# Kernel tuning notes

Measured on AMD Instinct MI355X. Metric: run time of the kernel, lower is better.

Reference implementation:

```python
import jax, jax.numpy as jnp
import numpy as np

B, S, D = 8, 2048, 512

def setup_inputs() -> dict:
    key = jax.random.key(0)
    k1, k2, k3 = jax.random.split(key, 3)
    context = jax.random.normal(k1, (B, S, D), dtype=jnp.float32)
    # nn.Linear default init ~ U(-1/sqrt(D), 1/sqrt(D)); scale keeps softmax sane
    bound = 1.0 / np.sqrt(D)
    W_in = jax.random.uniform(k2, (D, D), dtype=jnp.float32, minval=-bound, maxval=bound)
    W_out = jax.random.uniform(k3, (D, D), dtype=jnp.float32, minval=-bound, maxval=bound)
    return {"context": context, "W_in": W_in, "W_out": W_out}

def reference(context, W_in, W_out):
    # linear_in: x @ W_in.T (torch Linear convention)
    c = jnp.einsum('bsd,ed->bse', context, W_in)            # [B,S,D]
    scores = jnp.einsum('bsd,btd->bst', c, c)               # [B,S,S], no 1/sqrt(d) scale
    attn = jax.nn.softmax(scores, axis=-1)                  # [B,S,S]
    ctx = jnp.einsum('bst,btd->bsd', attn, c)               # [B,S,D]
    out = jnp.einsum('bsd,ed->bse', jnp.tanh(ctx), W_out)   # linear_out
    return out, attn
```

## Files before the change

### kernel.cpp

```cpp
#include <hip/hip_runtime.h>
#include <cstdint>
#include <cstddef>

#define Bc 8
#define Sc 2048
#define Dc 512

typedef float f32x4 __attribute__((ext_vector_type(4)));
typedef __bf16 bf16x8 __attribute__((ext_vector_type(8)));
typedef __bf16 bf16x4 __attribute__((ext_vector_type(4)));

__device__ __forceinline__ void gload_lds16(const void* g, void* l) {
    __builtin_amdgcn_global_load_lds((const __attribute__((address_space(1))) void*)g,
                                     (__attribute__((address_space(3))) void*)l, 16, 0, 0);
}

__device__ __forceinline__ f32x4 mfma16x16x32(bf16x8 a, bf16x8 b, f32x4 c) {
    return __builtin_amdgcn_mfma_f32_16x16x32_bf16(a, b, c, 0, 0, 0);
}

__global__ void k_convert_w(const float* __restrict__ wi, const float* __restrict__ wo,
                            __bf16* __restrict__ wib, __bf16* __restrict__ wob) {
    int i = blockIdx.x * 256 + threadIdx.x;
    wib[i] = (__bf16)wi[i];
    wob[i] = (__bf16)wo[i];
}

__global__ __launch_bounds__(256) void k_scores(
        const __bf16* __restrict__ c, __bf16* __restrict__ Ebuf,
        float2* __restrict__ stats)
{
    __shared__ alignas(16) char smem[34816];
    __bf16* As = (__bf16*)smem;
    __bf16* Bs = (__bf16*)(smem + 16384);
    const int tid  = threadIdx.x;
    const int wave = tid >> 6, lane = tid & 63;
    const int waveM = wave >> 1, waveN = wave & 1;
    const int bid  = blockIdx.x;
    const int bz   = bid & 7;
    const int col0 = ((bid >> 3) & 15) * 128;
    const int row0 = (bid >> 7) * 128;
    const __bf16* A  = c + (size_t)bz * Sc * Dc;

    f32x4 acc[4][4] = {};

    for (int k0 = 0; k0 < Dc; k0 += 64) {
        #pragma unroll
        for (int i = 0; i < 4; ++i) {
            int flat = i * 2048 + wave * 512 + lane * 8;
            int r  = flat >> 6;
            int cc = (flat >> 3) & 7;
            int gc = (cc ^ (r & 7)) << 3;
            gload_lds16(A + (size_t)(row0 + r) * Dc + k0 + gc, As + i * 2048 + wave * 512);
            gload_lds16(A + (size_t)(col0 + r) * Dc + k0 + gc, Bs + i * 2048 + wave * 512);
        }
        __syncthreads();
        #pragma unroll
        for (int ks = 0; ks < 2; ++ks) {
            const int kc = ks * 4 + (lane >> 4);
            bf16x8 av[4], bv[4];
            #pragma unroll
            for (int mi = 0; mi < 4; ++mi) {
                int r = waveM * 64 + mi * 16 + (lane & 15);
                av[mi] = *(const bf16x8*)&As[r * 64 + ((kc ^ (r & 7)) << 3)];
            }
            #pragma unroll
            for (int ni = 0; ni < 4; ++ni) {
                int r = waveN * 64 + ni * 16 + (lane & 15);
                bv[ni] = *(const bf16x8*)&Bs[r * 64 + ((kc ^ (r & 7)) << 3)];
            }
            #pragma unroll
            for (int mi = 0; mi < 4; ++mi)
                #pragma unroll
                for (int ni = 0; ni < 4; ++ni)
                    acc[mi][ni] = mfma16x16x32(av[mi], bv[ni], acc[mi][ni]);
        }
        __syncthreads();
    }

    const int rb = (lane >> 4) << 2;
    const int cb = lane & 15;
    __bf16* Es = (__bf16*)smem;
    #pragma unroll
    for (int mi = 0; mi < 4; ++mi)
        #pragma unroll
        for (int rr = 0; rr < 4; ++rr) {
            float mx = fmaxf(fmaxf(acc[mi][0][rr], acc[mi][1][rr]),
                             fmaxf(acc[mi][2][rr], acc[mi][3][rr]));
            #pragma unroll
            for (int off = 1; off < 16; off <<= 1) mx = fmaxf(mx, __shfl_xor(mx, off));
            const int rloc = waveM * 64 + mi * 16 + rb + rr;
            float zs = 0.f;
            #pragma unroll
            for (int ni = 0; ni < 4; ++ni) {
                float e = __expf(acc[mi][ni][rr] - mx);
                zs += e;
                Es[rloc * 136 + waveN * 64 + ni * 16 + cb] = (__bf16)e;
            }
            #pragma unroll
            for (int off = 1; off < 16; off <<= 1) zs += __shfl_xor(zs, off);
            if ((lane & 15) == 0)
                stats[((size_t)bz * Sc + row0 + rloc) * 32 + (col0 >> 6) + waveN] =
                    make_float2(mx, zs);
        }
    __syncthreads();
    #pragma unroll
    for (int p = 0; p < 8; ++p) {
        int r  = p * 16 + (tid >> 4);
        int cc = (tid & 15) * 8;
        bf16x8 v = *(const bf16x8*)&Es[r * 136 + cc];
        *(bf16x8*)&Ebuf[((size_t)bz * Sc + row0 + r) * Sc + col0 + cc] = v;
    }
}

__global__ __launch_bounds__(256) void k_combine(const float2* __restrict__ stats,
                                                 float* __restrict__ corrTab) {
    int r = blockIdx.x * 256 + threadIdx.x;
    float2 s[32];
    #pragma unroll
    for (int i = 0; i < 32; ++i) s[i] = stats[(size_t)r * 32 + i];
    float M = s[0].x;
    #pragma unroll
    for (int i = 1; i < 32; ++i) M = fmaxf(M, s[i].x);
    float Z = 0.f;
    #pragma unroll
    for (int i = 0; i < 32; ++i) Z += s[i].y * __expf(s[i].x - M);
    float zi = 1.f / Z;
    #pragma unroll
    for (int i = 0; i < 32; ++i) corrTab[(size_t)r * 32 + i] = __expf(s[i].x - M) * zi;
}

__global__ __launch_bounds__(512, 4) void k_pv_fused(
        const __bf16* __restrict__ Buf,
        const __bf16* __restrict__ cT,
        const float* __restrict__ corrTab,
        float* __restrict__ attn,
        __bf16* __restrict__ ctx)
{
    __shared__ alignas(16) __bf16 As[32 * 64];
    __shared__ alignas(16) __bf16 Bs[512 * 64];
    const int tid  = threadIdx.x;
    const int wave = tid >> 6, lane = tid & 63;
    const int b    = blockIdx.x & 7;
    const int row0 = (blockIdx.x >> 3) * 32;
    const __bf16* Bt = cT + (size_t)b * Dc * Sc;

    const int ar = tid >> 4;
    const int ac = (tid & 15) * 4;
    const __bf16* erow = Buf + ((size_t)b * Sc + row0 + ar) * Sc + ac;
    const float*  crow = corrTab + ((size_t)b * Sc + row0 + ar) * 32;
    float*        prow = attn + ((size_t)b * Sc + row0 + ar) * Sc + ac;
    const int a_addr = ar * 64 + (((ac >> 3) ^ (ar & 7)) << 3) + (ac & 4);

    f32x4 acc[2][4] = {};
    const int NT = Sc / 64;

    auto stageB = [&](int kt) {
        #pragma unroll
        for (int i = 0; i < 8; ++i) {
            int chunk = i * 512 + wave * 64 + lane;
            int r  = chunk >> 3;
            int cc = chunk & 7;
            gload_lds16(Bt + (size_t)r * Sc + kt + ((cc ^ (r & 7)) << 3),
                        Bs + (size_t)chunk * 8);
        }
    };

    bf16x4 e_cur = *(const bf16x4*)&erow[0];
    float  c_cur = crow[0];

    for (int t = 0; t < NT; ++t) {
        stageB(t * 64);
        f32x4 p;
        #pragma unroll
        for (int j = 0; j < 4; ++j) p[j] = (float)e_cur[j] * c_cur;
        bf16x4 pb;
        #pragma unroll
        for (int j = 0; j < 4; ++j) pb[j] = (__bf16)p[j];
        *(bf16x4*)&As[a_addr] = pb;
        __syncthreads();
        *(f32x4*)&prow[t * 64] = p;
        if (t + 1 < NT) {
            e_cur = *(const bf16x4*)&erow[(t + 1) * 64];
            c_cur = crow[t + 1];
        }
        const int kcb = lane >> 4;
        #pragma unroll
        for (int ks = 0; ks < 2; ++ks) {
            const int kc = ks * 4 + kcb;
            bf16x8 av[2], bv[4];
            #pragma unroll
            for (int mi = 0; mi < 2; ++mi) {
                int r = mi * 16 + (lane & 15);
                av[mi] = *(const bf16x8*)&As[r * 64 + ((kc ^ (r & 7)) << 3)];
            }
            #pragma unroll
            for (int ni = 0; ni < 4; ++ni) {
                int r = wave * 64 + ni * 16 + (lane & 15);
                bv[ni] = *(const bf16x8*)&Bs[r * 64 + ((kc ^ (r & 7)) << 3)];
            }
            #pragma unroll
            for (int mi = 0; mi < 2; ++mi)
                #pragma unroll
                for (int ni = 0; ni < 4; ++ni)
                    acc[mi][ni] = mfma16x16x32(av[mi], bv[ni], acc[mi][ni]);
        }
        __syncthreads();
    }

    const int rb = (lane >> 4) << 2;
    const int cb = lane & 15;
    #pragma unroll
    for (int mi = 0; mi < 2; ++mi)
        #pragma unroll
        for (int ni = 0; ni < 4; ++ni) {
            int gr = row0 + mi * 16 + rb;
            int gc = wave * 64 + ni * 16 + cb;
            #pragma unroll
            for (int rr = 0; rr < 4; ++rr)
                ctx[(size_t)(b * Sc + gr + rr) * Dc + gc] = (__bf16)tanhf(acc[mi][ni][rr]);
        }
}

__global__ __launch_bounds__(256) void k_gemm_bf16(
        const __bf16* __restrict__ A, const __bf16* __restrict__ Bt,
        float* __restrict__ C, int lda, int ldb, int ldc, int K)
{
    __shared__ alignas(16) __bf16 smem[2 * 128 * 64];
    __bf16* As = smem;
    __bf16* Bs = smem + 128 * 64;
    const int tid  = threadIdx.x;
    const int wave = tid >> 6, lane = tid & 63;
    const int waveM = wave >> 1, waveN = wave & 1;
    const int row0 = blockIdx.y * 128;
    const int col0 = blockIdx.x * 128;

    f32x4 acc[4][4] = {};

    for (int k0 = 0; k0 < K; k0 += 64) {
        #pragma unroll
        for (int i = 0; i < 4; ++i) {
            int flat = i * 2048 + wave * 512 + lane * 8;
            int r  = flat >> 6;
            int cc = (flat >> 3) & 7;
            int gc = (cc ^ (r & 7)) << 3;
            gload_lds16(A  + (size_t)(row0 + r) * lda + k0 + gc, As + i * 2048 + wave * 512);
            gload_lds16(Bt + (size_t)(col0 + r) * ldb + k0 + gc, Bs + i * 2048 + wave * 512);
        }
        __syncthreads();
        #pragma unroll
        for (int ks = 0; ks < 2; ++ks) {
            const int kc = ks * 4 + (lane >> 4);
            bf16x8 av[4], bv[4];
            #pragma unroll
            for (int mi = 0; mi < 4; ++mi) {
                int r = waveM * 64 + mi * 16 + (lane & 15);
                av[mi] = *(const bf16x8*)&As[r * 64 + ((kc ^ (r & 7)) << 3)];
            }
            #pragma unroll
            for (int ni = 0; ni < 4; ++ni) {
                int r = waveN * 64 + ni * 16 + (lane & 15);
                bv[ni] = *(const bf16x8*)&Bs[r * 64 + ((kc ^ (r & 7)) << 3)];
            }
            #pragma unroll
            for (int mi = 0; mi < 4; ++mi)
                #pragma unroll
                for (int ni = 0; ni < 4; ++ni)
                    acc[mi][ni] = mfma16x16x32(av[mi], bv[ni], acc[mi][ni]);
        }
        __syncthreads();
    }

    const int rb = (lane >> 4) << 2;
    const int cb = lane & 15;
    #pragma unroll
    for (int mi = 0; mi < 4; ++mi)
        #pragma unroll
        for (int ni = 0; ni < 4; ++ni) {
            int gr = row0 + waveM * 64 + mi * 16 + rb;
            int gc = col0 + waveN * 64 + ni * 16 + cb;
            #pragma unroll
            for (int rr = 0; rr < 4; ++rr)
                C[(size_t)(gr + rr) * ldc + gc] = acc[mi][ni][rr];
        }
}

__global__ __launch_bounds__(256) void k_cproj(
        const float* __restrict__ A, const __bf16* __restrict__ Bt,
        __bf16* __restrict__ Cb, __bf16* __restrict__ CTb)
{
    __shared__ alignas(16) char smem[49152];
    float*  Asf = (float*)smem;
    __bf16* Bs  = (__bf16*)(smem + 32768);
    const int tid  = threadIdx.x;
    const int wave = tid >> 6, lane = tid & 63;
    const int waveM = wave >> 1, waveN = wave & 1;
    const int row0 = blockIdx.y * 128;
    const int col0 = blockIdx.x * 128;

    f32x4 acc[4][4] = {};

    for (int k0 = 0; k0 < Dc; k0 += 64) {
        #pragma unroll
        for (int i = 0; i < 8; ++i) {
            int flat = i * 1024 + wave * 256 + lane * 4;
            int r  = flat >> 6;
            int cc = (flat >> 2) & 15;
            int gc = (cc ^ (r & 15)) << 2;
            gload_lds16(A + (size_t)(row0 + r) * Dc + k0 + gc, Asf + i * 1024 + wave * 256);
        }
        #pragma unroll
        for (int i = 0; i < 4; ++i) {
            int flat = i * 2048 + wave * 512 + lane * 8;
            int r  = flat >> 6;
            int cc = (flat >> 3) & 7;
            int gc = (cc ^ (r & 7)) << 3;
            gload_lds16(Bt + (size_t)(col0 + r) * Dc + k0 + gc, Bs + i * 2048 + wave * 512);
        }
        __syncthreads();
        #pragma unroll
        for (int ks = 0; ks < 2; ++ks) {
            const int kc8 = ks * 4 + (lane >> 4);
            const int kc4 = kc8 << 1;
            bf16x8 av[4], bv[4];
            #pragma unroll
            for (int mi = 0; mi < 4; ++mi) {
                int r  = waveM * 64 + mi * 16 + (lane & 15);
                int r4 = r & 15;
                f32x4 lo = *(const f32x4*)&Asf[r * 64 + (((kc4    ) ^ r4) << 2)];
                f32x4 hi = *(const f32x4*)&Asf[r * 64 + (((kc4 + 1) ^ r4) << 2)];
                bf16x8 a;
                a[0] = (__bf16)lo[0]; a[1] = (__bf16)lo[1]; a[2] = (__bf16)lo[2]; a[3] = (__bf16)lo[3];
                a[4] = (__bf16)hi[0]; a[5] = (__bf16)hi[1]; a[6] = (__bf16)hi[2]; a[7] = (__bf16)hi[3];
                av[mi] = a;
            }
            #pragma unroll
            for (int ni = 0; ni < 4; ++ni) {
                int r = waveN * 64 + ni * 16 + (lane & 15);
                bv[ni] = *(const bf16x8*)&Bs[r * 64 + ((kc8 ^ (r & 7)) << 3)];
            }
            #pragma unroll
            for (int mi = 0; mi < 4; ++mi)
                #pragma unroll
                for (int ni = 0; ni < 4; ++ni)
                    acc[mi][ni] = mfma16x16x32(av[mi], bv[ni], acc[mi][ni]);
        }
        __syncthreads();
    }

    const int rb = (lane >> 4) << 2;
    const int cb = lane & 15;
    __bf16* T = (__bf16*)smem;
    #pragma unroll
    for (int mi = 0; mi < 4; ++mi)
        #pragma unroll
        for (int ni = 0; ni < 4; ++ni) {
            int lr = waveM * 64 + mi * 16 + rb;
            int lc = waveN * 64 + ni * 16 + cb;
            #pragma unroll
            for (int rr = 0; rr < 4; ++rr) {
                __bf16 h = (__bf16)acc[mi][ni][rr];
                Cb[(size_t)(row0 + lr + rr) * Dc + col0 + lc] = h;
                T[lc * 136 + lr + rr] = h;
            }
        }
    __syncthreads();
    const int bb = row0 >> 11;
    const int s0 = row0 & 2047;
    #pragma unroll
    for (int i = 0; i < 8; ++i) {
        int n  = i * 16 + (tid >> 4);
        int mo = (tid & 15) * 8;
        bf16x8 v = *(const bf16x8*)&T[n * 136 + mo];
        *(bf16x8*)&CTb[(size_t)bb * Dc * Sc + (size_t)(col0 + n) * Sc + s0 + mo] = v;
    }
}

extern "C" void kernel_launch(void* const* d_in, const int* in_sizes, int n_in,
                              void* d_out, int out_size, void* d_ws, size_t ws_size,
                              hipStream_t stream)
{
    (void)in_sizes; (void)n_in; (void)out_size; (void)ws_size;
    const float* context = (const float*)d_in[0];
    const float* W_in    = (const float*)d_in[1];
    const float* W_out   = (const float*)d_in[2];
    float* out  = (float*)d_out;
    float* attn = out + (size_t)Bc * Sc * Dc;

    char* ws = (char*)d_ws;
    __bf16* c_bf    = (__bf16*)ws;
    __bf16* cT_bf   = (__bf16*)(ws + 16777216);
    __bf16* wi_bf   = (__bf16*)(ws + 33554432);
    __bf16* wo_bf   = (__bf16*)(ws + 34078720);
    float2* stats   = (float2*)(ws + 34603008);
    float*  corrTab = (float*)(ws + 38797312);
    __bf16* Ebuf    = (__bf16*)(ws + 40894464);

    k_convert_w<<<dim3(Dc * Dc / 256), 256, 0, stream>>>(W_in, W_out, wi_bf, wo_bf);

    k_cproj<<<dim3(Dc / 128, (Bc * Sc) / 128), 256, 0, stream>>>(context, wi_bf, c_bf, cT_bf);

    k_scores<<<dim3(Bc * 16 * 16), 256, 0, stream>>>(c_bf, Ebuf, stats);

    k_combine<<<dim3(Bc * Sc / 256), 256, 0, stream>>>(stats, corrTab);

    k_pv_fused<<<dim3((Sc / 32) * Bc), 512, 0, stream>>>(Ebuf, cT_bf, corrTab, attn, c_bf);

    k_gemm_bf16<<<dim3(Dc / 128, (Bc * Sc) / 128, 1), 256, 0, stream>>>(
        c_bf, wo_bf, out, Dc, Dc, Dc, Dc);
}
```

Measured before the change: 189.7 us.

## Pre-convert context to bf16 and retile PV kernel into 64-row, half-D blocks

Adds a separate pass that converts the fp32 context to bf16, so the projection GEMM stages bf16 tiles directly instead of fp32 tiles converted in registers. The fused PV kernel is retiled from 32 rows by the full D with 512 threads to 64 rows by half of D with 256 threads. Only the first half-D block writes the attn output, and each block reads the E rows once per 256 columns. The aim is a lower LDS footprint and more MFMA work per staged B tile, at the cost of an extra 32MB of traffic for the conversion and reading Ebuf twice.

```diff
diff --git a/kernel.cpp b/kernel.cpp
--- a/kernel.cpp
+++ b/kernel.cpp
@@ -24,6 +24,96 @@
     int i = blockIdx.x * 256 + threadIdx.x;
     wib[i] = (__bf16)wi[i];
     wob[i] = (__bf16)wo[i];
+}
+
+__global__ __launch_bounds__(256) void k_convert_x(const float* __restrict__ x,
+                                                   __bf16* __restrict__ xb) {
+    size_t base = ((size_t)blockIdx.x * 256 + threadIdx.x) * 16;
+    #pragma unroll
+    for (int j = 0; j < 4; ++j) {
+        f32x4 v = *(const f32x4*)&x[base + j * 4];
+        bf16x4 h;
+        #pragma unroll
+        for (int k = 0; k < 4; ++k) h[k] = (__bf16)v[k];
+        *(bf16x4*)&xb[base + j * 4] = h;
+    }
+}
+
+__global__ __launch_bounds__(256) void k_cproj(
+        const __bf16* __restrict__ Xb, const __bf16* __restrict__ Wt,
+        __bf16* __restrict__ Cb, __bf16* __restrict__ CTb)
+{
+    __shared__ alignas(16) char smem[34816];
+    __bf16* As = (__bf16*)smem;
+    __bf16* Bs = (__bf16*)(smem + 16384);
+    const int tid  = threadIdx.x;
+    const int wave = tid >> 6, lane = tid & 63;
+    const int waveM = wave >> 1, waveN = wave & 1;
+    const int row0 = blockIdx.y * 128;
+    const int col0 = blockIdx.x * 128;
+
+    f32x4 acc[4][4] = {};
+
+    for (int k0 = 0; k0 < Dc; k0 += 64) {
+        #pragma unroll
+        for (int i = 0; i < 4; ++i) {
+            int flat = i * 2048 + wave * 512 + lane * 8;
+            int r  = flat >> 6;
+            int cc = (flat >> 3) & 7;
+            int gc = (cc ^ (r & 7)) << 3;
+            gload_lds16(Xb + (size_t)(row0 + r) * Dc + k0 + gc, As + i * 2048 + wave * 512);
+            gload_lds16(Wt + (size_t)(col0 + r) * Dc + k0 + gc, Bs + i * 2048 + wave * 512);
+        }
+        __syncthreads();
+        #pragma unroll
+        for (int ks = 0; ks < 2; ++ks) {
+            const int kc = ks * 4 + (lane >> 4);
+            bf16x8 av[4], bv[4];
+            #pragma unroll
+            for (int mi = 0; mi < 4; ++mi) {
+                int r = waveM * 64 + mi * 16 + (lane & 15);
+                av[mi] = *(const bf16x8*)&As[r * 64 + ((kc ^ (r & 7)) << 3)];
+            }
+            #pragma unroll
+            for (int ni = 0; ni < 4; ++ni) {
+                int r = waveN * 64 + ni * 16 + (lane & 15);
+                bv[ni] = *(const bf16x8*)&Bs[r * 64 + ((kc ^ (r & 7)) << 3)];
+            }
+            #pragma unroll
+            for (int mi = 0; mi < 4; ++mi)
+                #pragma unroll
+                for (int ni = 0; ni < 4; ++ni)
+                    acc[mi][ni] = mfma16x16x32(av[mi], bv[ni], acc[mi][ni]);
+        }
+        __syncthreads();
+    }
+
+    const int rb = (lane >> 4) << 2;
+    const int cb = lane & 15;
+    __bf16* T = (__bf16*)smem;
+    #pragma unroll
+    for (int mi = 0; mi < 4; ++mi)
+        #pragma unroll
+        for (int ni = 0; ni < 4; ++ni) {
+            int lr = waveM * 64 + mi * 16 + rb;
+            int lc = waveN * 64 + ni * 16 + cb;
+            #pragma unroll
+            for (int rr = 0; rr < 4; ++rr) {
+                __bf16 h = (__bf16)acc[mi][ni][rr];
+                Cb[(size_t)(row0 + lr + rr) * Dc + col0 + lc] = h;
+                T[lc * 136 + lr + rr] = h;
+            }
+        }
+    __syncthreads();
+    const int bb = row0 >> 11;
+    const int s0 = row0 & 2047;
+    #pragma unroll
+    for (int i = 0; i < 8; ++i) {
+        int n  = i * 16 + (tid >> 4);
+        int mo = (tid & 15) * 8;
+        bf16x8 v = *(const bf16x8*)&T[n * 136 + mo];
+        *(bf16x8*)&CTb[(size_t)bb * Dc * Sc + (size_t)(col0 + n) * Sc + s0 + mo] = v;
+    }
 }
 
 __global__ __launch_bounds__(256) void k_scores(
@@ -130,35 +220,40 @@
     for (int i = 0; i < 32; ++i) corrTab[(size_t)r * 32 + i] = __expf(s[i].x - M) * zi;
 }
 
-__global__ __launch_bounds__(512, 4) void k_pv_fused(
-        const __bf16* __restrict__ Buf,
+__global__ __launch_bounds__(256, 2) void k_pv_fused(
+        const __bf16* __restrict__ Ebuf,
         const __bf16* __restrict__ cT,
         const float* __restrict__ corrTab,
         float* __restrict__ attn,
         __bf16* __restrict__ ctx)
 {
-    __shared__ alignas(16) __bf16 As[32 * 64];
-    __shared__ alignas(16) __bf16 Bs[512 * 64];
+    __shared__ alignas(16) __bf16 As[64 * 64];
+    __shared__ alignas(16) __bf16 Bs[256 * 64];
     const int tid  = threadIdx.x;
     const int wave = tid >> 6, lane = tid & 63;
-    const int b    = blockIdx.x & 7;
-    const int row0 = (blockIdx.x >> 3) * 32;
-    const __bf16* Bt = cT + (size_t)b * Dc * Sc;
-
-    const int ar = tid >> 4;
-    const int ac = (tid & 15) * 4;
-    const __bf16* erow = Buf + ((size_t)b * Sc + row0 + ar) * Sc + ac;
+    const int bid  = blockIdx.x;
+    const int b      = bid & 7;
+    const int row0   = ((bid >> 3) & 31) * 64;
+    const int dhalf  = bid >> 8;
+    const int d0     = dhalf * 256;
+    const __bf16* Bt = cT + (size_t)b * Dc * Sc + (size_t)d0 * Sc;
+
+    const int ar = tid >> 2;
+    const int ac = (tid & 3) * 16;
+    const __bf16* erow = Ebuf + ((size_t)b * Sc + row0 + ar) * Sc + ac;
     const float*  crow = corrTab + ((size_t)b * Sc + row0 + ar) * 32;
     float*        prow = attn + ((size_t)b * Sc + row0 + ar) * Sc + ac;
-    const int a_addr = ar * 64 + (((ac >> 3) ^ (ar & 7)) << 3) + (ac & 4);
-
-    f32x4 acc[2][4] = {};
+    const int c8 = (tid & 3) * 2;
+    const int a_addr0 = ar * 64 + ((c8 ^ (ar & 7)) << 3);
+    const int a_addr1 = ar * 64 + (((c8 + 1) ^ (ar & 7)) << 3);
+
+    f32x4 acc[4][4] = {};
     const int NT = Sc / 64;
 
     auto stageB = [&](int kt) {
         #pragma unroll
         for (int i = 0; i < 8; ++i) {
-            int chunk = i * 512 + wave * 64 + lane;
+            int chunk = i * 256 + tid;
             int r  = chunk >> 3;
             int cc = chunk & 7;
             gload_lds16(Bt + (size_t)r * Sc + kt + ((cc ^ (r & 7)) << 3),
@@ -166,31 +261,46 @@
         }
     };
 
-    bf16x4 e_cur = *(const bf16x4*)&erow[0];
-    float  c_cur = crow[0];
+    bf16x8 e0 = *(const bf16x8*)&erow[0];
+    bf16x8 e1 = *(const bf16x8*)&erow[8];
+    float  cc_ = crow[0];
 
     for (int t = 0; t < NT; ++t) {
         stageB(t * 64);
-        f32x4 p;
-        #pragma unroll
-        for (int j = 0; j < 4; ++j) p[j] = (float)e_cur[j] * c_cur;
-        bf16x4 pb;
-        #pragma unroll
-        for (int j = 0; j < 4; ++j) pb[j] = (__bf16)p[j];
-        *(bf16x4*)&As[a_addr] = pb;
-        __syncthreads();
-        *(f32x4*)&prow[t * 64] = p;
+        f32x4 p0, p1, p2, p3;
+        #pragma unroll
+        for (int j = 0; j < 4; ++j) {
+            p0[j] = (float)e0[j]     * cc_;
+            p1[j] = (float)e0[4 + j] * cc_;
+            p2[j] = (float)e1[j]     * cc_;
+            p3[j] = (float)e1[4 + j] * cc_;
+        }
+        bf16x8 pa, pb;
+        #pragma unroll
+        for (int j = 0; j < 4; ++j) {
+            pa[j] = (__bf16)p0[j]; pa[4 + j] = (__bf16)p1[j];
+            pb[j] = (__bf16)p2[j]; pb[4 + j] = (__bf16)p3[j];
+        }
+        *(bf16x8*)&As[a_addr0] = pa;
+        *(bf16x8*)&As[a_addr1] = pb;
+        __syncthreads();
+        if (dhalf == 0) {
+            *(f32x4*)&prow[t * 64]      = p0;
+            *(f32x4*)&prow[t * 64 + 4]  = p1;
+            *(f32x4*)&prow[t * 64 + 8]  = p2;
+            *(f32x4*)&prow[t * 64 + 12] = p3;
+        }
         if (t + 1 < NT) {
-            e_cur = *(const bf16x4*)&erow[(t + 1) * 64];
-            c_cur = crow[t + 1];
-        }
-        const int kcb = lane >> 4;
+            e0  = *(const bf16x8*)&erow[(t + 1) * 64];
+            e1  = *(const bf16x8*)&erow[(t + 1) * 64 + 8];
+            cc_ = crow[t + 1];
+        }
         #pragma unroll
         for (int ks = 0; ks < 2; ++ks) {
-            const int kc = ks * 4 + kcb;
-            bf16x8 av[2], bv[4];
-            #pragma unroll
-            for (int mi = 0; mi < 2; ++mi) {
+            const int kc = ks * 4 + (lane >> 4);
+            bf16x8 av[4], bv[4];
+            #pragma unroll
+            for (int mi = 0; mi < 4; ++mi) {
                 int r = mi * 16 + (lane & 15);
                 av[mi] = *(const bf16x8*)&As[r * 64 + ((kc ^ (r & 7)) << 3)];
             }
@@ -200,7 +310,7 @@
                 bv[ni] = *(const bf16x8*)&Bs[r * 64 + ((kc ^ (r & 7)) << 3)];
             }
             #pragma unroll
-            for (int mi = 0; mi < 2; ++mi)
+            for (int mi = 0; mi < 4; ++mi)
                 #pragma unroll
                 for (int ni = 0; ni < 4; ++ni)
                     acc[mi][ni] = mfma16x16x32(av[mi], bv[ni], acc[mi][ni]);
@@ -211,11 +321,11 @@
     const int rb = (lane >> 4) << 2;
     const int cb = lane & 15;
     #pragma unroll
-    for (int mi = 0; mi < 2; ++mi)
+    for (int mi = 0; mi < 4; ++mi)
         #pragma unroll
         for (int ni = 0; ni < 4; ++ni) {
             int gr = row0 + mi * 16 + rb;
-            int gc = wave * 64 + ni * 16 + cb;
+            int gc = d0 + wave * 64 + ni * 16 + cb;
             #pragma unroll
             for (int rr = 0; rr < 4; ++rr)
                 ctx[(size_t)(b * Sc + gr + rr) * Dc + gc] = (__bf16)tanhf(acc[mi][ni][rr]);
@@ -285,97 +395,6 @@
         }
 }
 
-__global__ __launch_bounds__(256) void k_cproj(
-        const float* __restrict__ A, const __bf16* __restrict__ Bt,
-        __bf16* __restrict__ Cb, __bf16* __restrict__ CTb)
-{
-    __shared__ alignas(16) char smem[49152];
-    float*  Asf = (float*)smem;
-    __bf16* Bs  = (__bf16*)(smem + 32768);
-    const int tid  = threadIdx.x;
-    const int wave = tid >> 6, lane = tid & 63;
-    const int waveM = wave >> 1, waveN = wave & 1;
-    const int row0 = blockIdx.y * 128;
-    const int col0 = blockIdx.x * 128;
-
-    f32x4 acc[4][4] = {};
-
-    for (int k0 = 0; k0 < Dc; k0 += 64) {
-        #pragma unroll
-        for (int i = 0; i < 8; ++i) {
-            int flat = i * 1024 + wave * 256 + lane * 4;
-            int r  = flat >> 6;
-            int cc = (flat >> 2) & 15;
-            int gc = (cc ^ (r & 15)) << 2;
-            gload_lds16(A + (size_t)(row0 + r) * Dc + k0 + gc, Asf + i * 1024 + wave * 256);
-        }
-        #pragma unroll
-        for (int i = 0; i < 4; ++i) {
-            int flat = i * 2048 + wave * 512 + lane * 8;
-            int r  = flat >> 6;
-            int cc = (flat >> 3) & 7;
-            int gc = (cc ^ (r & 7)) << 3;
-            gload_lds16(Bt + (size_t)(col0 + r) * Dc + k0 + gc, Bs + i * 2048 + wave * 512);
-        }
-        __syncthreads();
-        #pragma unroll
-        for (int ks = 0; ks < 2; ++ks) {
-            const int kc8 = ks * 4 + (lane >> 4);
-            const int kc4 = kc8 << 1;
-            bf16x8 av[4], bv[4];
-            #pragma unroll
-            for (int mi = 0; mi < 4; ++mi) {
-                int r  = waveM * 64 + mi * 16 + (lane & 15);
-                int r4 = r & 15;
-                f32x4 lo = *(const f32x4*)&Asf[r * 64 + (((kc4    ) ^ r4) << 2)];
-                f32x4 hi = *(const f32x4*)&Asf[r * 64 + (((kc4 + 1) ^ r4) << 2)];
-                bf16x8 a;
-                a[0] = (__bf16)lo[0]; a[1] = (__bf16)lo[1]; a[2] = (__bf16)lo[2]; a[3] = (__bf16)lo[3];
-                a[4] = (__bf16)hi[0]; a[5] = (__bf16)hi[1]; a[6] = (__bf16)hi[2]; a[7] = (__bf16)hi[3];
-                av[mi] = a;
-            }
-            #pragma unroll
-            for (int ni = 0; ni < 4; ++ni) {
-                int r = waveN * 64 + ni * 16 + (lane & 15);
-                bv[ni] = *(const bf16x8*)&Bs[r * 64 + ((kc8 ^ (r & 7)) << 3)];
-            }
-            #pragma unroll
-            for (int mi = 0; mi < 4; ++mi)
-                #pragma unroll
-                for (int ni = 0; ni < 4; ++ni)
-                    acc[mi][ni] = mfma16x16x32(av[mi], bv[ni], acc[mi][ni]);
-        }
-        __syncthreads();
-    }
-
-    const int rb = (lane >> 4) << 2;
-    const int cb = lane & 15;
-    __bf16* T = (__bf16*)smem;
-    #pragma unroll
-    for (int mi = 0; mi < 4; ++mi)
-        #pragma unroll
-        for (int ni = 0; ni < 4; ++ni) {
-            int lr = waveM * 64 + mi * 16 + rb;
-            int lc = waveN * 64 + ni * 16 + cb;
-            #pragma unroll
-            for (int rr = 0; rr < 4; ++rr) {
-                __bf16 h = (__bf16)acc[mi][ni][rr];
-                Cb[(size_t)(row0 + lr + rr) * Dc + col0 + lc] = h;
-                T[lc * 136 + lr + rr] = h;
-            }
-        }
-    __syncthreads();
-    const int bb = row0 >> 11;
-    const int s0 = row0 & 2047;
-    #pragma unroll
-    for (int i = 0; i < 8; ++i) {
-        int n  = i * 16 + (tid >> 4);
-        int mo = (tid & 15) * 8;
-        bf16x8 v = *(const bf16x8*)&T[n * 136 + mo];
-        *(bf16x8*)&CTb[(size_t)bb * Dc * Sc + (size_t)(col0 + n) * Sc + s0 + mo] = v;
-    }
-}
-
 extern "C" void kernel_launch(void* const* d_in, const int* in_sizes, int n_in,
                               void* d_out, int out_size, void* d_ws, size_t ws_size,
                               hipStream_t stream)
@@ -395,16 +414,18 @@
     float2* stats   = (float2*)(ws + 34603008);
     float*  corrTab = (float*)(ws + 38797312);
     __bf16* Ebuf    = (__bf16*)(ws + 40894464);
+    __bf16* x_bf    = (__bf16*)(ws + 40894464 + 67108864);
 
     k_convert_w<<<dim3(Dc * Dc / 256), 256, 0, stream>>>(W_in, W_out, wi_bf, wo_bf);
-
-    k_cproj<<<dim3(Dc / 128, (Bc * Sc) / 128), 256, 0, stream>>>(context, wi_bf, c_bf, cT_bf);
+    k_convert_x<<<dim3((Bc * Sc * Dc) / (256 * 16)), 256, 0, stream>>>(context, x_bf);
+
+    k_cproj<<<dim3(Dc / 128, (Bc * Sc) / 128), 256, 0, stream>>>(x_bf, wi_bf, c_bf, cT_bf);
 
     k_scores<<<dim3(Bc * 16 * 16), 256, 0, stream>>>(c_bf, Ebuf, stats);
 
     k_combine<<<dim3(Bc * Sc / 256), 256, 0, stream>>>(stats, corrTab);
 
-    k_pv_fused<<<dim3((Sc / 32) * Bc), 512, 0, stream>>>(Ebuf, cT_bf, corrTab, attn, c_bf);
+    k_pv_fused<<<dim3(512), 256, 0, stream>>>(Ebuf, cT_bf, corrTab, attn, c_bf);
 
     k_gemm_bf16<<<dim3(Dc / 128, (Bc * Sc) / 128, 1), 256, 0, stream>>>(
         c_bf, wo_bf, out, Dc, Dc, Dc, Dc);
```

New measurement: 203.1 us. 7.1% more time.

## Double M-tile in PV kernel and software-pipeline B staging with MFMA

Applied to the files above, without the earlier changes.

The fused PV kernel now handles 64 query rows per block instead of 32, which halves how often the cT tile is reloaded for each row of output. The main loop is restructured so all LDS fragments are read into registers first, then the next B tile is issued with async global-to-LDS loads and the next probability tile is written, overlapping with the MFMAs. Explicit waitcnt and s_barrier calls replace the two __syncthreads per iteration. The cost is higher register pressure (16 accumulator tiles plus prefetched fragments, with the occupancy hint dropped) and half as many blocks.

```diff
diff --git a/kernel.cpp b/kernel.cpp
--- a/kernel.cpp
+++ b/kernel.cpp
@@ -130,35 +130,35 @@
     for (int i = 0; i < 32; ++i) corrTab[(size_t)r * 32 + i] = __expf(s[i].x - M) * zi;
 }
 
-__global__ __launch_bounds__(512, 4) void k_pv_fused(
-        const __bf16* __restrict__ Buf,
+__global__ __launch_bounds__(512) void k_pv_fused(
+        const __bf16* __restrict__ Ebuf,
         const __bf16* __restrict__ cT,
         const float* __restrict__ corrTab,
         float* __restrict__ attn,
         __bf16* __restrict__ ctx)
 {
-    __shared__ alignas(16) __bf16 As[32 * 64];
+    __shared__ alignas(16) __bf16 As[64 * 64];
     __shared__ alignas(16) __bf16 Bs[512 * 64];
     const int tid  = threadIdx.x;
     const int wave = tid >> 6, lane = tid & 63;
     const int b    = blockIdx.x & 7;
-    const int row0 = (blockIdx.x >> 3) * 32;
+    const int row0 = (blockIdx.x >> 3) * 64;
     const __bf16* Bt = cT + (size_t)b * Dc * Sc;
 
-    const int ar = tid >> 4;
-    const int ac = (tid & 15) * 4;
-    const __bf16* erow = Buf + ((size_t)b * Sc + row0 + ar) * Sc + ac;
+    const int ar = tid >> 3;
+    const int ac = (tid & 7) * 8;
+    const __bf16* erow = Ebuf + ((size_t)b * Sc + row0 + ar) * Sc + ac;
     const float*  crow = corrTab + ((size_t)b * Sc + row0 + ar) * 32;
     float*        prow = attn + ((size_t)b * Sc + row0 + ar) * Sc + ac;
-    const int a_addr = ar * 64 + (((ac >> 3) ^ (ar & 7)) << 3) + (ac & 4);
-
-    f32x4 acc[2][4] = {};
+    const int a_addr = ar * 64 + (((ac >> 3) ^ (ar & 7)) << 3);
+
+    f32x4 acc[4][4] = {};
     const int NT = Sc / 64;
 
     auto stageB = [&](int kt) {
         #pragma unroll
         for (int i = 0; i < 8; ++i) {
-            int chunk = i * 512 + wave * 64 + lane;
+            int chunk = i * 512 + tid;
             int r  = chunk >> 3;
             int cc = chunk & 7;
             gload_lds16(Bt + (size_t)r * Sc + kt + ((cc ^ (r & 7)) << 3),
@@ -166,52 +166,89 @@
         }
     };
 
-    bf16x4 e_cur = *(const bf16x4*)&erow[0];
-    float  c_cur = crow[0];
+    bf16x8 e = *(const bf16x8*)&erow[0];
+    float  cf = crow[0];
+    f32x4 p0, p1;
+    #pragma unroll
+    for (int j = 0; j < 4; ++j) { p0[j] = (float)e[j] * cf; p1[j] = (float)e[4 + j] * cf; }
+    {
+        bf16x8 pb;
+        #pragma unroll
+        for (int j = 0; j < 4; ++j) { pb[j] = (__bf16)p0[j]; pb[4 + j] = (__bf16)p1[j]; }
+        *(bf16x8*)&As[a_addr] = pb;
+    }
+    stageB(0);
+    __builtin_amdgcn_sched_barrier(0);
+    *(f32x4*)&prow[0] = p0;
+    *(f32x4*)&prow[4] = p1;
+    e  = *(const bf16x8*)&erow[64];
+    cf = crow[1];
+    asm volatile("s_waitcnt vmcnt(4) lgkmcnt(0)" ::: "memory");
+    __builtin_amdgcn_sched_barrier(0);
+    __builtin_amdgcn_s_barrier();
 
     for (int t = 0; t < NT; ++t) {
-        stageB(t * 64);
-        f32x4 p;
-        #pragma unroll
-        for (int j = 0; j < 4; ++j) p[j] = (float)e_cur[j] * c_cur;
-        bf16x4 pb;
-        #pragma unroll
-        for (int j = 0; j < 4; ++j) pb[j] = (__bf16)p[j];
-        *(bf16x4*)&As[a_addr] = pb;
-        __syncthreads();
-        *(f32x4*)&prow[t * 64] = p;
-        if (t + 1 < NT) {
-            e_cur = *(const bf16x4*)&erow[(t + 1) * 64];
-            c_cur = crow[t + 1];
-        }
-        const int kcb = lane >> 4;
+        bf16x8 av[4][2], bv[2][4];
         #pragma unroll
         for (int ks = 0; ks < 2; ++ks) {
-            const int kc = ks * 4 + kcb;
-            bf16x8 av[2], bv[4];
-            #pragma unroll
-            for (int mi = 0; mi < 2; ++mi) {
+            const int kc = ks * 4 + (lane >> 4);
+            #pragma unroll
+            for (int mi = 0; mi < 4; ++mi) {
                 int r = mi * 16 + (lane & 15);
-                av[mi] = *(const bf16x8*)&As[r * 64 + ((kc ^ (r & 7)) << 3)];
+                av[mi][ks] = *(const bf16x8*)&As[r * 64 + ((kc ^ (r & 7)) << 3)];
             }
             #pragma unroll
             for (int ni = 0; ni < 4; ++ni) {
                 int r = wave * 64 + ni * 16 + (lane & 15);
-                bv[ni] = *(const bf16x8*)&Bs[r * 64 + ((kc ^ (r & 7)) << 3)];
-            }
-            #pragma unroll
-            for (int mi = 0; mi < 2; ++mi)
+                bv[ks][ni] = *(const bf16x8*)&Bs[r * 64 + ((kc ^ (r & 7)) << 3)];
+            }
+        }
+        asm volatile("s_waitcnt lgkmcnt(0)" ::: "memory");
+        __builtin_amdgcn_sched_barrier(0);
+        __builtin_amdgcn_s_barrier();
+
+        if (t + 1 < NT) {
+            stageB((t + 1) * 64);
+            __builtin_amdgcn_sched_barrier(0);
+            f32x4 q0, q1;
+            #pragma unroll
+            for (int j = 0; j < 4; ++j) {
+                q0[j] = (float)e[j] * cf; q1[j] = (float)e[4 + j] * cf;
+            }
+            bf16x8 pb;
+            #pragma unroll
+            for (int j = 0; j < 4; ++j) { pb[j] = (__bf16)q0[j]; pb[4 + j] = (__bf16)q1[j]; }
+            *(bf16x8*)&As[a_addr] = pb;
+            *(f32x4*)&prow[(t + 1) * 64]     = q0;
+            *(f32x4*)&prow[(t + 1) * 64 + 4] = q1;
+            if (t + 2 < NT) {
+                e  = *(const bf16x8*)&erow[(t + 2) * 64];
+                cf = crow[t + 2];
+            }
+        }
+
+        #pragma unroll
+        for (int ks = 0; ks < 2; ++ks)
+            #pragma unroll
+            for (int mi = 0; mi < 4; ++mi)
                 #pragma unroll
                 for (int ni = 0; ni < 4; ++ni)
-                    acc[mi][ni] = mfma16x16x32(av[mi], bv[ni], acc[mi][ni]);
-        }
-        __syncthreads();
+                    acc[mi][ni] = mfma16x16x32(av[mi][ks], bv[ks][ni], acc[mi][ni]);
+
+        if (t + 1 < NT) {
+            if (t + 2 < NT)
+                asm volatile("s_waitcnt vmcnt(4) lgkmcnt(0)" ::: "memory");
+            else
+                asm volatile("s_waitcnt vmcnt(2) lgkmcnt(0)" ::: "memory");
+            __builtin_amdgcn_sched_barrier(0);
+            __builtin_amdgcn_s_barrier();
+        }
     }
 
     const int rb = (lane >> 4) << 2;
     const int cb = lane & 15;
     #pragma unroll
-    for (int mi = 0; mi < 2; ++mi)
+    for (int mi = 0; mi < 4; ++mi)
         #pragma unroll
         for (int ni = 0; ni < 4; ++ni) {
             int gr = row0 + mi * 16 + rb;
@@ -404,7 +441,7 @@
 
     k_combine<<<dim3(Bc * Sc / 256), 256, 0, stream>>>(stats, corrTab);
 
-    k_pv_fused<<<dim3((Sc / 32) * Bc), 512, 0, stream>>>(Ebuf, cT_bf, corrTab, attn, c_bf);
+    k_pv_fused<<<dim3((Sc / 64) * Bc), 512, 0, stream>>>(Ebuf, cT_bf, corrTab, attn, c_bf);
 
     k_gemm_bf16<<<dim3(Dc / 128, (Bc * Sc) / 128, 1), 256, 0, stream>>>(
         c_bf, wo_bf, out, Dc, Dc, Dc, Dc);
```

Measured after the change: 185.4 us, median of 2. 2.2% less time.
